# Optimization experiments

Measured on AMD Instinct MI355X. Metric: run time of the kernel, lower is better.

Reference implementation:

```python
import jax, jax.numpy as jnp
import numpy as np
from jax import lax

IN_CHANNELS = 64
OUT_CHANNELS = 192
REP = OUT_CHANNELS // 6  # 32 identical output channels per direction

# Six fixed directional 3x3 stencils (same as the torch module).
_STENCILS = np.array([
    [[1., 0., 0.], [0., 1., 0.], [0., 0., 1.]],  # main diagonal
    [[0., 0., 1.], [0., 1., 0.], [1., 0., 0.]],  # anti-diagonal
    [[1., 0., 1.], [0., 1., 0.], [1., 0., 1.]],  # X
    [[0., 1., 0.], [1., 1., 1.], [0., 1., 0.]],  # +
    [[0., 0., 0.], [1., 1., 1.], [0., 0., 0.]],  # horizontal
    [[0., 1., 0.], [0., 1., 0.], [0., 1., 0.]],  # vertical
], dtype=np.float32)
STENCILS = jnp.asarray(_STENCILS)[:, None, :, :]  # (6, 1, 3, 3) OIHW


def setup_inputs() -> dict:
    key = jax.random.key(0)
    x = jax.random.normal(key, (8, IN_CHANNELS, 256, 256), dtype=jnp.float32)
    return {"x": x}


def reference(x) -> jnp.ndarray:
    # Each torch conv uses the SAME 3x3 stencil for every (out_ch, in_ch) pair,
    # so out[b,o] = stencil * sum_c x[b,c], identical across the REP out channels.
    # Compute each directional map once on the channel-summed input, then broadcast.
    xs = jnp.sum(x, axis=1, keepdims=True)  # (B, 1, H, W)
    y = lax.conv_general_dilated(
        xs, STENCILS,
        window_strides=(1, 1), padding=((1, 1), (1, 1)),
        dimension_numbers=("NCHW", "OIHW", "NCHW"),
    )  # (B, 6, H, W)
    # torch.cat([x1..x6], dim=1): REP copies of dir0, then REP of dir1, ...
    out = jnp.repeat(y, REP, axis=1)  # (B, OUT_CHANNELS, H, W)
    return jax.nn.relu(out)
```

## Files before the change

### kernel.cpp

```cpp
#include <hip/hip_runtime.h>

typedef float f32x4 __attribute__((ext_vector_type(4)));

constexpr int B = 8, C = 64, H = 256, W = 256;
constexpr int HW = H * W;
constexpr int HW4 = HW / 4;
constexpr int W4 = W / 4;
constexpr int OUTC = 192;

__global__ __launch_bounds__(256) void chansum_k(const float* __restrict__ x,
                                                 float* __restrict__ S) {
    int tid = blockIdx.x * 256 + threadIdx.x;
    int b = tid >> 14;
    int hw4 = tid & (HW4 - 1);
    const f32x4* xp = (const f32x4*)x + (size_t)b * C * HW4 + hw4;
    f32x4 a0 = 0, a1 = 0, a2 = 0, a3 = 0;
#pragma unroll
    for (int c = 0; c < C; c += 4) {
        f32x4 v0 = __builtin_nontemporal_load(xp + (size_t)(c + 0) * HW4);
        f32x4 v1 = __builtin_nontemporal_load(xp + (size_t)(c + 1) * HW4);
        f32x4 v2 = __builtin_nontemporal_load(xp + (size_t)(c + 2) * HW4);
        f32x4 v3 = __builtin_nontemporal_load(xp + (size_t)(c + 3) * HW4);
        a0 += v0; a1 += v1; a2 += v2; a3 += v3;
    }
    f32x4 s = (a0 + a1) + (a2 + a3);
    ((f32x4*)S)[(size_t)b * HW4 + hw4] = s;
}

__global__ __launch_bounds__(256) void stencil_oc_k(const float* __restrict__ S,
                                                    float* __restrict__ out) {
    int tid = blockIdx.x * 256 + threadIdx.x;
    int w4 = tid & (W4 - 1);
    int t = tid >> 6;
    int h = t & (H - 1);
    int boc = t >> 8;
    int b = boc / 192;
    int d = (boc - b * 192) >> 5;
    int w0 = w4 << 2;

    const float* Sb = S + (size_t)b * HW;
    f32x4 cc[3];
    float ll[3], rr[3];
#pragma unroll
    for (int i = 0; i < 3; ++i) {
        int hh = h - 1 + i;
        if (hh < 0 || hh >= H) {
            cc[i] = 0; ll[i] = 0.f; rr[i] = 0.f;
        } else {
            const float* row = Sb + hh * W + w0;
            cc[i] = *(const f32x4*)row;
            ll[i] = (w0 > 0)     ? row[-1] : 0.f;
            rr[i] = (w0 + 4 < W) ? row[4]  : 0.f;
        }
    }
    f32x4 m1[3], p1[3];
#pragma unroll
    for (int i = 0; i < 3; ++i) {
        m1[i] = (f32x4){ ll[i],    cc[i][0], cc[i][1], cc[i][2] };
        p1[i] = (f32x4){ cc[i][1], cc[i][2], cc[i][3], rr[i]    };
    }

    f32x4 v;
    if      (d == 0) v = m1[0] + cc[1] + p1[2];
    else if (d == 1) v = p1[0] + cc[1] + m1[2];
    else if (d == 2) v = (m1[0] + p1[0]) + cc[1] + (m1[2] + p1[2]);
    else if (d == 3) v = cc[0] + (m1[1] + cc[1] + p1[1]) + cc[2];
    else if (d == 4) v = m1[1] + cc[1] + p1[1];
    else             v = cc[0] + cc[1] + cc[2];

    v = (f32x4){ fmaxf(v[0], 0.f), fmaxf(v[1], 0.f),
                 fmaxf(v[2], 0.f), fmaxf(v[3], 0.f) };

    float* op = out + (size_t)boc * HW + h * W + w0;
    __builtin_nontemporal_store(v, (f32x4*)op);
}

extern "C" void kernel_launch(void* const* d_in, const int* in_sizes, int n_in,
                              void* d_out, int out_size, void* d_ws, size_t ws_size,
                              hipStream_t stream) {
    const float* x = (const float*)d_in[0];
    float* out = (float*)d_out;
    float* S = (float*)d_ws;

    chansum_k<<<(B * HW4) / 256, 256, 0, stream>>>(x, S);
    stencil_oc_k<<<(B * OUTC * H * W4) / 256, 256, 0, stream>>>(S, out);
}
```

Before: 572.3 us.

## Compute each stencil once per direction and replicate across 32 output channels

The stencil kernel now computes each directional result once per (batch, direction) for a 4-row by 4-column tile and writes it to all 32 replicated output channels, instead of recomputing per output channel. Horizontal neighbours come from wave shuffles instead of extra scalar loads. Nontemporal loads and stores are replaced by plain ones in both kernels. This removes redundant reads of S and stencil arithmetic, but each thread now issues 128 strided stores, which may affect store coalescing and occupancy.

Measured after the change: 499.0 us. -12.8%, faster.

```diff
diff --git a/kernel.cpp b/kernel.cpp
--- a/kernel.cpp
+++ b/kernel.cpp
@@ -17,62 +17,70 @@
     f32x4 a0 = 0, a1 = 0, a2 = 0, a3 = 0;
 #pragma unroll
     for (int c = 0; c < C; c += 4) {
-        f32x4 v0 = __builtin_nontemporal_load(xp + (size_t)(c + 0) * HW4);
-        f32x4 v1 = __builtin_nontemporal_load(xp + (size_t)(c + 1) * HW4);
-        f32x4 v2 = __builtin_nontemporal_load(xp + (size_t)(c + 2) * HW4);
-        f32x4 v3 = __builtin_nontemporal_load(xp + (size_t)(c + 3) * HW4);
-        a0 += v0; a1 += v1; a2 += v2; a3 += v3;
+        a0 += xp[(size_t)(c + 0) * HW4];
+        a1 += xp[(size_t)(c + 1) * HW4];
+        a2 += xp[(size_t)(c + 2) * HW4];
+        a3 += xp[(size_t)(c + 3) * HW4];
     }
-    f32x4 s = (a0 + a1) + (a2 + a3);
-    ((f32x4*)S)[(size_t)b * HW4 + hw4] = s;
+    ((f32x4*)S)[(size_t)b * HW4 + hw4] = (a0 + a1) + (a2 + a3);
 }
 
-__global__ __launch_bounds__(256) void stencil_oc_k(const float* __restrict__ S,
-                                                    float* __restrict__ out) {
+__global__ __launch_bounds__(256) void stencil4_k(const float* __restrict__ S,
+                                                  float* __restrict__ out) {
     int tid = blockIdx.x * 256 + threadIdx.x;
-    int w4 = tid & (W4 - 1);
-    int t = tid >> 6;
-    int h = t & (H - 1);
-    int boc = t >> 8;
-    int b = boc / 192;
-    int d = (boc - b * 192) >> 5;
+    int w4 = tid & 63;
+    int hg = (tid >> 6) & 63;
+    int rest = tid >> 12;
+    int d = rest % 6;
+    int b = rest / 6;
     int w0 = w4 << 2;
+    int h0 = hg << 2;
 
     const float* Sb = S + (size_t)b * HW;
-    f32x4 cc[3];
-    float ll[3], rr[3];
+
+    f32x4 cc[6];
 #pragma unroll
-    for (int i = 0; i < 3; ++i) {
-        int hh = h - 1 + i;
-        if (hh < 0 || hh >= H) {
-            cc[i] = 0; ll[i] = 0.f; rr[i] = 0.f;
-        } else {
-            const float* row = Sb + hh * W + w0;
-            cc[i] = *(const f32x4*)row;
-            ll[i] = (w0 > 0)     ? row[-1] : 0.f;
-            rr[i] = (w0 + 4 < W) ? row[4]  : 0.f;
-        }
+    for (int i = 0; i < 6; ++i) {
+        int hh = h0 - 1 + i;
+        cc[i] = (hh < 0 || hh >= H) ? (f32x4)0 : *(const f32x4*)(Sb + hh * W + w0);
     }
-    f32x4 m1[3], p1[3];
+    float ll[6], rr[6];
 #pragma unroll
-    for (int i = 0; i < 3; ++i) {
+    for (int i = 0; i < 6; ++i) {
+        float lv = __shfl_up(cc[i][3], 1);
+        float rv = __shfl_down(cc[i][0], 1);
+        ll[i] = (w4 == 0)  ? 0.f : lv;
+        rr[i] = (w4 == 63) ? 0.f : rv;
+    }
+    f32x4 m1[6], p1[6];
+#pragma unroll
+    for (int i = 0; i < 6; ++i) {
         m1[i] = (f32x4){ ll[i],    cc[i][0], cc[i][1], cc[i][2] };
         p1[i] = (f32x4){ cc[i][1], cc[i][2], cc[i][3], rr[i]    };
     }
 
-    f32x4 v;
-    if      (d == 0) v = m1[0] + cc[1] + p1[2];
-    else if (d == 1) v = p1[0] + cc[1] + m1[2];
-    else if (d == 2) v = (m1[0] + p1[0]) + cc[1] + (m1[2] + p1[2]);
-    else if (d == 3) v = cc[0] + (m1[1] + cc[1] + p1[1]) + cc[2];
-    else if (d == 4) v = m1[1] + cc[1] + p1[1];
-    else             v = cc[0] + cc[1] + cc[2];
+    f32x4 res[4];
+#pragma unroll
+    for (int j = 0; j < 4; ++j) {
+        f32x4 v;
+        if      (d == 0) v = m1[j] + cc[j+1] + p1[j+2];
+        else if (d == 1) v = p1[j] + cc[j+1] + m1[j+2];
+        else if (d == 2) v = (m1[j] + p1[j]) + cc[j+1] + (m1[j+2] + p1[j+2]);
+        else if (d == 3) v = cc[j] + (m1[j+1] + cc[j+1] + p1[j+1]) + cc[j+2];
+        else if (d == 4) v = m1[j+1] + cc[j+1] + p1[j+1];
+        else             v = cc[j] + cc[j+1] + cc[j+2];
+        res[j] = (f32x4){ fmaxf(v[0], 0.f), fmaxf(v[1], 0.f),
+                          fmaxf(v[2], 0.f), fmaxf(v[3], 0.f) };
+    }
 
-    v = (f32x4){ fmaxf(v[0], 0.f), fmaxf(v[1], 0.f),
-                 fmaxf(v[2], 0.f), fmaxf(v[3], 0.f) };
-
-    float* op = out + (size_t)boc * HW + h * W + w0;
-    __builtin_nontemporal_store(v, (f32x4*)op);
+    float* base = out + (size_t)(b * OUTC + d * 32) * HW + h0 * W + w0;
+#pragma unroll
+    for (int r = 0; r < 32; ++r) {
+        float* op = base + (size_t)r * HW;
+#pragma unroll
+        for (int j = 0; j < 4; ++j)
+            *(f32x4*)(op + j * W) = res[j];
+    }
 }
 
 extern "C" void kernel_launch(void* const* d_in, const int* in_sizes, int n_in,
@@ -83,5 +91,5 @@
     float* S = (float*)d_ws;
 
     chansum_k<<<(B * HW4) / 256, 256, 0, stream>>>(x, S);
-    stencil_oc_k<<<(B * OUTC * H * W4) / 256, 256, 0, stream>>>(S, out);
+    stencil4_k<<<(B * 6 * 64 * 64) / 256, 256, 0, stream>>>(S, out);
 }
```
